# Kernel tuning notes

Hardware: AMD Instinct MI355X
Metric: run time of the kernel (lower is better)

The kernel has to match this reference:

```python
import jax, jax.numpy as jnp
import numpy as np

NUM_VARS = 22
LAYERS = 2
N = 2 ** NUM_VARS


def setup_inputs() -> dict:
    key = jax.random.key(0)
    k1, k2, k3, k4 = jax.random.split(key, 4)
    h = jax.random.normal(k1, (N,), dtype=jnp.float32)          # unsatisfied-clause 'energy' per bitstring
    hS = jax.random.uniform(k2, (N,), dtype=jnp.float32)        # satisfiability weight per bitstring
    gamma = jax.random.normal(k3, (LAYERS,), dtype=jnp.float32) * 0.01
    beta = jax.random.normal(k4, (LAYERS,), dtype=jnp.float32) * 0.01
    return {"h": h, "hS": hS, "gamma": gamma, "beta": beta}


def reference(h, hS, gamma, beta):
    n = NUM_VARS
    # |+>^n initial state: uniform amplitudes 1/sqrt(N)
    circuit = jnp.full((N,), 1.0 / np.sqrt(N), dtype=jnp.complex64)
    for l in range(LAYERS):
        # cost unitary: elementwise phase exp(i * gamma * h)
        circuit = jnp.exp((1j * gamma[l] * h).astype(jnp.complex64)) * circuit
        # mixing unitary: per-qubit X-rotation butterfly.
        # torch's transpose(0,i)+split+cat swaps the two slices along qubit axis i,
        # which for a size-2 axis is exactly a flip along that axis.
        cb = jnp.cos(beta[l]).astype(jnp.complex64)
        sb = (1j * jnp.sin(beta[l])).astype(jnp.complex64)
        c = circuit.reshape((2,) * n)
        for i in range(n):  # fixed small loop over qubits (structurally distinct axes)
            c = cb * c + sb * jnp.flip(c, axis=i)
        circuit = c.reshape(N)
    ps = jnp.real(circuit * jnp.conj(circuit))  # |amplitude|^2
    return jnp.dot(ps, hS)
```

## Files before the change

### kernel.cpp

```cpp
#include <hip/hip_runtime.h>


#define NTOT    (1u << 22)
#define LO_BITS 13
#define HI_BITS 9
#define LO      (1u << LO_BITS)
#define HI      (1u << HI_BITS)
#define GRP     16
#define TPB     512
#define R       16

#define REGSTAGE(MASK, CB, SB) {                                  \
    _Pragma("unroll")                                             \
    for (int r0 = 0; r0 < R; ++r0) {                              \
        if ((r0 & (MASK)) == 0) {                                 \
            const int r1 = r0 | (MASK);                           \
            float t0r = re[r0], t0i = im[r0];                     \
            float t1r = re[r1], t1i = im[r1];                     \
            re[r0] = (CB) * t0r - (SB) * t1i;                     \
            im[r0] = (CB) * t0i + (SB) * t1r;                     \
            re[r1] = (CB) * t1r - (SB) * t0i;                     \
            im[r1] = (CB) * t1i + (SB) * t0r;                     \
        } } }

#define SHFLSTAGE(MASK, CB, SB) {                                 \
    _Pragma("unroll")                                             \
    for (int r = 0; r < R; ++r) {                                 \
        float tr = re[r], ti = im[r];                             \
        float pr = __shfl_xor(tr, (MASK), 64);                    \
        float pi = __shfl_xor(ti, (MASK), 64);                    \
        re[r] = (CB) * tr - (SB) * pi;                            \
        im[r] = (CB) * ti + (SB) * pr;                            \
    } }

__global__ __launch_bounds__(TPB, 4) void k_init_low(
    const float* __restrict__ h, const float* __restrict__ gam,
    const float* __restrict__ bet, float2* __restrict__ st)
{
    __shared__ float2 sC[LO];
    const float g1 = gam[0];
    const float cb = __cosf(bet[0]), sb = __sinf(bet[0]);
    const unsigned t = threadIdx.x, lane = t & 63u, wave = t >> 6;
    const size_t base = (size_t)blockIdx.x * LO;
    float re[R], im[R];

    #pragma unroll
    for (int r = 0; r < R; ++r) {
        float s, c;
        __sincosf(g1 * h[base + (unsigned)r * TPB + t], &s, &c);
        re[r] = c * 0x1p-11f;
        im[r] = s * 0x1p-11f;
    }
    REGSTAGE(1, cb, sb)  REGSTAGE(2, cb, sb)
    REGSTAGE(4, cb, sb)  REGSTAGE(8, cb, sb)
    SHFLSTAGE(1,  cb, sb) SHFLSTAGE(2,  cb, sb)
    SHFLSTAGE(4,  cb, sb) SHFLSTAGE(8,  cb, sb)
    SHFLSTAGE(16, cb, sb) SHFLSTAGE(32, cb, sb)
    #pragma unroll
    for (int r = 0; r < R; ++r) sC[(unsigned)r * TPB + t] = make_float2(re[r], im[r]);
    __syncthreads();
    #pragma unroll
    for (int r = 0; r < R; ++r) {
        unsigned j = lane | ((unsigned)(r & 7) << 6) | (wave << 9) | ((unsigned)(r >> 3) << 12);
        float2 v = sC[j]; re[r] = v.x; im[r] = v.y;
    }
    REGSTAGE(1, cb, sb)  REGSTAGE(2, cb, sb)
    REGSTAGE(4, cb, sb)
    #pragma unroll
    for (int r = 0; r < R; ++r) {
        unsigned j = lane | ((unsigned)(r & 7) << 6) | (wave << 9) | ((unsigned)(r >> 3) << 12);
        st[base + j] = make_float2(re[r], im[r]);
    }
}

__global__ __launch_bounds__(TPB, 4) void k_high(
    const float* __restrict__ h, const float* __restrict__ gam,
    const float* __restrict__ bet, float2* __restrict__ st)
{
    __shared__ float2 sC[GRP * HI];
    const float g2  = gam[1];
    const float cb1 = __cosf(bet[0]), sb1 = __sinf(bet[0]);
    const float cb2 = __cosf(bet[1]), sb2 = __sinf(bet[1]);
    const unsigned t = threadIdx.x, lane = t & 63u, wave = t >> 6;
    const unsigned lo0 = blockIdx.x * GRP;
    const unsigned g   = lane & (GRP - 1);
    const unsigned h01 = lane >> 4;
    float re[R], im[R];

    #pragma unroll
    for (int r = 0; r < R; ++r) {
        unsigned hi = h01 | (wave << 2) | ((unsigned)r << 5);
        float2 v = st[(size_t)hi * LO + lo0 + g];
        re[r] = v.x; im[r] = v.y;
    }
    REGSTAGE(1, cb1, sb1)  REGSTAGE(2, cb1, sb1)
    REGSTAGE(4, cb1, sb1)  REGSTAGE(8, cb1, sb1)
    SHFLSTAGE(16, cb1, sb1) SHFLSTAGE(32, cb1, sb1)
    #pragma unroll
    for (int r = 0; r < R; ++r) {
        unsigned li = g | (h01 << 4) | (wave << 6) | ((unsigned)r << 9);
        sC[li] = make_float2(re[r], im[r]);
    }
    __syncthreads();
    #pragma unroll
    for (int r = 0; r < R; ++r) {
        unsigned li = g | (h01 << 4) | ((unsigned)(r & 7) << 6) | (wave << 9) | ((unsigned)(r >> 3) << 12);
        float2 v = sC[li]; re[r] = v.x; im[r] = v.y;
    }
    REGSTAGE(1, cb1, sb1)  REGSTAGE(2, cb1, sb1)  REGSTAGE(4, cb1, sb1)
    #pragma unroll
    for (int r = 0; r < R; ++r) {
        unsigned hi = h01 | ((unsigned)(r & 7) << 2) | (wave << 5) | ((unsigned)(r >> 3) << 8);
        float s, c;
        __sincosf(g2 * h[(size_t)hi * LO + lo0 + g], &s, &c);
        float tr = re[r], ti = im[r];
        re[r] = tr * c - ti * s;
        im[r] = tr * s + ti * c;
    }
    REGSTAGE(1, cb2, sb2)  REGSTAGE(2, cb2, sb2)
    REGSTAGE(4, cb2, sb2)  REGSTAGE(8, cb2, sb2)
    SHFLSTAGE(16, cb2, sb2) SHFLSTAGE(32, cb2, sb2)
    __syncthreads();
    #pragma unroll
    for (int r = 0; r < R; ++r) {
        unsigned li = g | (h01 << 4) | ((unsigned)(r & 7) << 6) | (wave << 9) | ((unsigned)(r >> 3) << 12);
        sC[li] = make_float2(re[r], im[r]);
    }
    __syncthreads();
    #pragma unroll
    for (int r = 0; r < R; ++r) {
        unsigned li = g | (h01 << 4) | (wave << 6) | ((unsigned)r << 9);
        float2 v = sC[li]; re[r] = v.x; im[r] = v.y;
    }
    REGSTAGE(1, cb2, sb2)  REGSTAGE(2, cb2, sb2)  REGSTAGE(4, cb2, sb2)
    #pragma unroll
    for (int r = 0; r < R; ++r) {
        unsigned hi = h01 | (wave << 2) | ((unsigned)r << 5);
        st[(size_t)hi * LO + lo0 + g] = make_float2(re[r], im[r]);
    }
}

__global__ __launch_bounds__(TPB, 4) void k_low2(
    const float* __restrict__ hS, const float* __restrict__ bet,
    const float2* __restrict__ st, float* __restrict__ partial)
{
    __shared__ float2 sC[LO];
    __shared__ float wsum[TPB / 64];
    const float cb = __cosf(bet[1]), sb = __sinf(bet[1]);
    const unsigned t = threadIdx.x, lane = t & 63u, wave = t >> 6;
    const size_t base = (size_t)blockIdx.x * LO;
    float re[R], im[R];

    #pragma unroll
    for (int r = 0; r < R; ++r) {
        float2 v = st[base + (unsigned)r * TPB + t];
        re[r] = v.x; im[r] = v.y;
    }
    REGSTAGE(1, cb, sb)  REGSTAGE(2, cb, sb)
    REGSTAGE(4, cb, sb)  REGSTAGE(8, cb, sb)
    SHFLSTAGE(1,  cb, sb) SHFLSTAGE(2,  cb, sb)
    SHFLSTAGE(4,  cb, sb) SHFLSTAGE(8,  cb, sb)
    SHFLSTAGE(16, cb, sb) SHFLSTAGE(32, cb, sb)
    #pragma unroll
    for (int r = 0; r < R; ++r) sC[(unsigned)r * TPB + t] = make_float2(re[r], im[r]);
    __syncthreads();
    #pragma unroll
    for (int r = 0; r < R; ++r) {
        unsigned j = lane | ((unsigned)(r & 7) << 6) | (wave << 9) | ((unsigned)(r >> 3) << 12);
        float2 v = sC[j]; re[r] = v.x; im[r] = v.y;
    }
    REGSTAGE(1, cb, sb)  REGSTAGE(2, cb, sb)  REGSTAGE(4, cb, sb)
    float acc = 0.f;
    #pragma unroll
    for (int r = 0; r < R; ++r) {
        unsigned j = lane | ((unsigned)(r & 7) << 6) | (wave << 9) | ((unsigned)(r >> 3) << 12);
        acc = fmaf(re[r] * re[r] + im[r] * im[r], hS[base + j], acc);
    }
    #pragma unroll
    for (int off = 32; off >= 1; off >>= 1)
        acc += __shfl_down(acc, off, 64);
    if (lane == 0) wsum[wave] = acc;
    __syncthreads();
    if (t == 0) {
        float s = 0.f;
        #pragma unroll
        for (int w = 0; w < TPB / 64; ++w) s += wsum[w];
        partial[blockIdx.x] = s;
    }
}

__global__ __launch_bounds__(TPB) void k_final(
    const float* __restrict__ partial, float* __restrict__ out)
{
    __shared__ float wsum[TPB / 64];
    const unsigned t = threadIdx.x;
    float acc = partial[t];
    #pragma unroll
    for (int off = 32; off >= 1; off >>= 1)
        acc += __shfl_down(acc, off, 64);
    if ((t & 63u) == 0u) wsum[t >> 6] = acc;
    __syncthreads();
    if (t == 0) {
        float s = 0.f;
        #pragma unroll
        for (int w = 0; w < TPB / 64; ++w) s += wsum[w];
        out[0] = s;
    }
}

extern "C" void kernel_launch(void* const* d_in, const int* in_sizes, int n_in,
                              void* d_out, int out_size, void* d_ws, size_t ws_size,
                              hipStream_t stream)
{
    (void)in_sizes; (void)n_in; (void)out_size; (void)ws_size;
    const float* h   = (const float*)d_in[0];
    const float* hS  = (const float*)d_in[1];
    const float* gam = (const float*)d_in[2];
    const float* bet = (const float*)d_in[3];
    float2* st     = (float2*)d_ws;
    float* partial = (float*)((char*)d_ws + (size_t)NTOT * sizeof(float2));
    float* out     = (float*)d_out;

    k_init_low<<<dim3(NTOT / LO), dim3(TPB), 0, stream>>>(h, gam, bet, st);
    k_high    <<<dim3(LO / GRP),  dim3(TPB), 0, stream>>>(h, gam, bet, st);
    k_low2    <<<dim3(NTOT / LO), dim3(TPB), 0, stream>>>(hS, bet, st, partial);
    k_final   <<<dim3(1),         dim3(TPB), 0, stream>>>(partial, out);
}
```

Before: 124.9 us.

## Store state in packed fp16 and replace final reduction kernel with atomics

The complex state vector is now held as packed half-precision pairs (RTZ conversion) in global memory, shared memory and cross-lane shuffles. This halves the workspace traffic and needs one shuffle per element instead of two. The separate final-reduction kernel is removed: each k_low2 block atomically adds its partial sum into the output, which k_init_low zeroes. The cost is heavy precision loss, since amplitudes near 2^-11 sit in the fp16 subnormal range with round-toward-zero, plus a float summation order that now depends on timing.

```diff
diff --git a/kernel.cpp b/kernel.cpp
--- a/kernel.cpp
+++ b/kernel.cpp
@@ -9,6 +9,16 @@
 #define GRP     16
 #define TPB     512
 #define R       16
+
+typedef __fp16 h2_t __attribute__((ext_vector_type(2)));
+union PkU { unsigned u; h2_t h; };
+
+__device__ __forceinline__ unsigned pk(float x, float y) {
+    PkU p; p.h = __builtin_amdgcn_cvt_pkrtz(x, y); return p.u;
+}
+__device__ __forceinline__ float2 unpk(unsigned v) {
+    PkU p; p.u = v; return make_float2((float)p.h.x, (float)p.h.y);
+}
 
 #define REGSTAGE(MASK, CB, SB) {                                  \
     _Pragma("unroll")                                             \
@@ -26,24 +36,27 @@
 #define SHFLSTAGE(MASK, CB, SB) {                                 \
     _Pragma("unroll")                                             \
     for (int r = 0; r < R; ++r) {                                 \
+        unsigned pv = (unsigned)__shfl_xor((int)pk(re[r], im[r]), (MASK), 64); \
+        float2 p = unpk(pv);                                      \
         float tr = re[r], ti = im[r];                             \
-        float pr = __shfl_xor(tr, (MASK), 64);                    \
-        float pi = __shfl_xor(ti, (MASK), 64);                    \
-        re[r] = (CB) * tr - (SB) * pi;                            \
-        im[r] = (CB) * ti + (SB) * pr;                            \
+        re[r] = (CB) * tr - (SB) * p.y;                           \
+        im[r] = (CB) * ti + (SB) * p.x;                           \
     } }
 
 __global__ __launch_bounds__(TPB, 4) void k_init_low(
     const float* __restrict__ h, const float* __restrict__ gam,
-    const float* __restrict__ bet, float2* __restrict__ st)
-{
-    __shared__ float2 sC[LO];
+    const float* __restrict__ bet, unsigned* __restrict__ st,
+    float* __restrict__ out)
+{
+    __shared__ unsigned sC[LO];
     const float g1 = gam[0];
     const float cb = __cosf(bet[0]), sb = __sinf(bet[0]);
     const unsigned t = threadIdx.x, lane = t & 63u, wave = t >> 6;
     const size_t base = (size_t)blockIdx.x * LO;
     float re[R], im[R];
 
+    if (blockIdx.x == 0 && t == 0) out[0] = 0.f;
+
     #pragma unroll
     for (int r = 0; r < R; ++r) {
         float s, c;
@@ -57,27 +70,26 @@
     SHFLSTAGE(4,  cb, sb) SHFLSTAGE(8,  cb, sb)
     SHFLSTAGE(16, cb, sb) SHFLSTAGE(32, cb, sb)
     #pragma unroll
-    for (int r = 0; r < R; ++r) sC[(unsigned)r * TPB + t] = make_float2(re[r], im[r]);
-    __syncthreads();
-    #pragma unroll
-    for (int r = 0; r < R; ++r) {
-        unsigned j = lane | ((unsigned)(r & 7) << 6) | (wave << 9) | ((unsigned)(r >> 3) << 12);
-        float2 v = sC[j]; re[r] = v.x; im[r] = v.y;
-    }
-    REGSTAGE(1, cb, sb)  REGSTAGE(2, cb, sb)
-    REGSTAGE(4, cb, sb)
-    #pragma unroll
-    for (int r = 0; r < R; ++r) {
-        unsigned j = lane | ((unsigned)(r & 7) << 6) | (wave << 9) | ((unsigned)(r >> 3) << 12);
-        st[base + j] = make_float2(re[r], im[r]);
+    for (int r = 0; r < R; ++r) sC[(unsigned)r * TPB + t] = pk(re[r], im[r]);
+    __syncthreads();
+    #pragma unroll
+    for (int r = 0; r < R; ++r) {
+        unsigned j = lane | ((unsigned)(r & 7) << 6) | (wave << 9) | ((unsigned)(r >> 3) << 12);
+        float2 v = unpk(sC[j]); re[r] = v.x; im[r] = v.y;
+    }
+    REGSTAGE(1, cb, sb)  REGSTAGE(2, cb, sb)  REGSTAGE(4, cb, sb)
+    #pragma unroll
+    for (int r = 0; r < R; ++r) {
+        unsigned j = lane | ((unsigned)(r & 7) << 6) | (wave << 9) | ((unsigned)(r >> 3) << 12);
+        st[base + j] = pk(re[r], im[r]);
     }
 }
 
 __global__ __launch_bounds__(TPB, 4) void k_high(
     const float* __restrict__ h, const float* __restrict__ gam,
-    const float* __restrict__ bet, float2* __restrict__ st)
-{
-    __shared__ float2 sC[GRP * HI];
+    const float* __restrict__ bet, unsigned* __restrict__ st)
+{
+    __shared__ unsigned sC[GRP * HI];
     const float g2  = gam[1];
     const float cb1 = __cosf(bet[0]), sb1 = __sinf(bet[0]);
     const float cb2 = __cosf(bet[1]), sb2 = __sinf(bet[1]);
@@ -90,7 +102,7 @@
     #pragma unroll
     for (int r = 0; r < R; ++r) {
         unsigned hi = h01 | (wave << 2) | ((unsigned)r << 5);
-        float2 v = st[(size_t)hi * LO + lo0 + g];
+        float2 v = unpk(st[(size_t)hi * LO + lo0 + g]);
         re[r] = v.x; im[r] = v.y;
     }
     REGSTAGE(1, cb1, sb1)  REGSTAGE(2, cb1, sb1)
@@ -99,13 +111,13 @@
     #pragma unroll
     for (int r = 0; r < R; ++r) {
         unsigned li = g | (h01 << 4) | (wave << 6) | ((unsigned)r << 9);
-        sC[li] = make_float2(re[r], im[r]);
+        sC[li] = pk(re[r], im[r]);
     }
     __syncthreads();
     #pragma unroll
     for (int r = 0; r < R; ++r) {
         unsigned li = g | (h01 << 4) | ((unsigned)(r & 7) << 6) | (wave << 9) | ((unsigned)(r >> 3) << 12);
-        float2 v = sC[li]; re[r] = v.x; im[r] = v.y;
+        float2 v = unpk(sC[li]); re[r] = v.x; im[r] = v.y;
     }
     REGSTAGE(1, cb1, sb1)  REGSTAGE(2, cb1, sb1)  REGSTAGE(4, cb1, sb1)
     #pragma unroll
@@ -124,27 +136,27 @@
     #pragma unroll
     for (int r = 0; r < R; ++r) {
         unsigned li = g | (h01 << 4) | ((unsigned)(r & 7) << 6) | (wave << 9) | ((unsigned)(r >> 3) << 12);
-        sC[li] = make_float2(re[r], im[r]);
+        sC[li] = pk(re[r], im[r]);
     }
     __syncthreads();
     #pragma unroll
     for (int r = 0; r < R; ++r) {
         unsigned li = g | (h01 << 4) | (wave << 6) | ((unsigned)r << 9);
-        float2 v = sC[li]; re[r] = v.x; im[r] = v.y;
+        float2 v = unpk(sC[li]); re[r] = v.x; im[r] = v.y;
     }
     REGSTAGE(1, cb2, sb2)  REGSTAGE(2, cb2, sb2)  REGSTAGE(4, cb2, sb2)
     #pragma unroll
     for (int r = 0; r < R; ++r) {
         unsigned hi = h01 | (wave << 2) | ((unsigned)r << 5);
-        st[(size_t)hi * LO + lo0 + g] = make_float2(re[r], im[r]);
+        st[(size_t)hi * LO + lo0 + g] = pk(re[r], im[r]);
     }
 }
 
 __global__ __launch_bounds__(TPB, 4) void k_low2(
     const float* __restrict__ hS, const float* __restrict__ bet,
-    const float2* __restrict__ st, float* __restrict__ partial)
-{
-    __shared__ float2 sC[LO];
+    const unsigned* __restrict__ st, float* __restrict__ out)
+{
+    __shared__ unsigned sC[LO];
     __shared__ float wsum[TPB / 64];
     const float cb = __cosf(bet[1]), sb = __sinf(bet[1]);
     const unsigned t = threadIdx.x, lane = t & 63u, wave = t >> 6;
@@ -153,7 +165,7 @@
 
     #pragma unroll
     for (int r = 0; r < R; ++r) {
-        float2 v = st[base + (unsigned)r * TPB + t];
+        float2 v = unpk(st[base + (unsigned)r * TPB + t]);
         re[r] = v.x; im[r] = v.y;
     }
     REGSTAGE(1, cb, sb)  REGSTAGE(2, cb, sb)
@@ -162,12 +174,12 @@
     SHFLSTAGE(4,  cb, sb) SHFLSTAGE(8,  cb, sb)
     SHFLSTAGE(16, cb, sb) SHFLSTAGE(32, cb, sb)
     #pragma unroll
-    for (int r = 0; r < R; ++r) sC[(unsigned)r * TPB + t] = make_float2(re[r], im[r]);
-    __syncthreads();
-    #pragma unroll
-    for (int r = 0; r < R; ++r) {
-        unsigned j = lane | ((unsigned)(r & 7) << 6) | (wave << 9) | ((unsigned)(r >> 3) << 12);
-        float2 v = sC[j]; re[r] = v.x; im[r] = v.y;
+    for (int r = 0; r < R; ++r) sC[(unsigned)r * TPB + t] = pk(re[r], im[r]);
+    __syncthreads();
+    #pragma unroll
+    for (int r = 0; r < R; ++r) {
+        unsigned j = lane | ((unsigned)(r & 7) << 6) | (wave << 9) | ((unsigned)(r >> 3) << 12);
+        float2 v = unpk(sC[j]); re[r] = v.x; im[r] = v.y;
     }
     REGSTAGE(1, cb, sb)  REGSTAGE(2, cb, sb)  REGSTAGE(4, cb, sb)
     float acc = 0.f;
@@ -185,26 +197,7 @@
         float s = 0.f;
         #pragma unroll
         for (int w = 0; w < TPB / 64; ++w) s += wsum[w];
-        partial[blockIdx.x] = s;
-    }
-}
-
-__global__ __launch_bounds__(TPB) void k_final(
-    const float* __restrict__ partial, float* __restrict__ out)
-{
-    __shared__ float wsum[TPB / 64];
-    const unsigned t = threadIdx.x;
-    float acc = partial[t];
-    #pragma unroll
-    for (int off = 32; off >= 1; off >>= 1)
-        acc += __shfl_down(acc, off, 64);
-    if ((t & 63u) == 0u) wsum[t >> 6] = acc;
-    __syncthreads();
-    if (t == 0) {
-        float s = 0.f;
-        #pragma unroll
-        for (int w = 0; w < TPB / 64; ++w) s += wsum[w];
-        out[0] = s;
+        unsafeAtomicAdd(out, s);
     }
 }
 
@@ -217,12 +210,10 @@
     const float* hS  = (const float*)d_in[1];
     const float* gam = (const float*)d_in[2];
     const float* bet = (const float*)d_in[3];
-    float2* st     = (float2*)d_ws;
-    float* partial = (float*)((char*)d_ws + (size_t)NTOT * sizeof(float2));
-    float* out     = (float*)d_out;
-
-    k_init_low<<<dim3(NTOT / LO), dim3(TPB), 0, stream>>>(h, gam, bet, st);
+    unsigned* st = (unsigned*)d_ws;
+    float* out   = (float*)d_out;
+
+    k_init_low<<<dim3(NTOT / LO), dim3(TPB), 0, stream>>>(h, gam, bet, st, out);
     k_high    <<<dim3(LO / GRP),  dim3(TPB), 0, stream>>>(h, gam, bet, st);
-    k_low2    <<<dim3(NTOT / LO), dim3(TPB), 0, stream>>>(hS, bet, st, partial);
-    k_final   <<<dim3(1),         dim3(TPB), 0, stream>>>(partial, out);
-}
+    k_low2    <<<dim3(NTOT / LO), dim3(TPB), 0, stream>>>(hS, bet, st, out);
+}
```

New measurement: 125.9 us. Within noise of the previous version (+0.8%).
